# Kernel optimization log

Hardware: AMD Instinct MI355X
Metric: run time of the kernel (lower is better)

Reference implementation:

```python
import jax, jax.numpy as jnp
import numpy as np

NBITS = 8
REDUCE = 64
OUT = 512


def setup_inputs() -> dict:
    key = jax.random.key(0)
    ks = jax.random.split(key, 6)
    T, B, C = 512, 16, 512
    ne = 2 ** NBITS
    x = jax.random.normal(ks[0], (T, B, C), dtype=jnp.float32)
    key_in = jax.random.normal(ks[1], (T, B, C), dtype=jnp.float32)  # unused by forward (overwritten)
    # xavier-ish init scales
    map_w = jax.random.normal(ks[2], (NBITS, C), dtype=jnp.float32) * np.sqrt(2.0 / (C + NBITS))
    map_b = jnp.zeros((NBITS,), dtype=jnp.float32)
    pw_w1 = jax.random.normal(ks[3], (REDUCE, C), dtype=jnp.float32) * np.sqrt(2.0 / (C + REDUCE))
    pw_w21 = jax.random.normal(ks[4], (ne, OUT * REDUCE), dtype=jnp.float32) * np.sqrt(2.0 / (ne + OUT * REDUCE))
    pw_w22 = jax.random.normal(ks[5], (ne, OUT * REDUCE), dtype=jnp.float32) * np.sqrt(2.0 / (ne + OUT * REDUCE))
    pw_B = jnp.zeros((1, 1, OUT), dtype=jnp.float32)
    return {"x": x, "key": key_in, "map_w": map_w, "map_b": map_b,
            "pw_w1": pw_w1, "pw_w21": pw_w21, "pw_w22": pw_w22, "pw_B": pw_B}


def reference(x, key, map_w, map_b, pw_w1, pw_w21, pw_w22, pw_B):
    # x: (T,B,C). `key` arg is overwritten by x in the original source.
    T, B, C = x.shape
    nbits = map_w.shape[0]
    out_dim = pw_B.shape[-1]
    reduce_dim = pw_w1.shape[0]

    k = x.reshape(T * B, C) @ map_w.T + map_b          # (T*B, nbits)
    z = jnp.clip(1.2 * jax.nn.sigmoid(k) - 0.1, 0.0, 1.0)  # saturated sigmoid
    code = (z > 0.5).astype(z.dtype)                   # eval: hard binary code

    pows = (2 ** jnp.arange(nbits, dtype=jnp.int32))   # bit_to_int weights
    qz1 = jnp.sum(code.astype(jnp.int32) * pows, axis=-1)          # (T*B,)
    qz2 = jnp.sum((1 - code.astype(jnp.int32)) * pows, axis=-1)    # (T*B,)

    # gather per-token expert rows and synthesize per-token weight matrix
    w2 = (pw_w21[qz1] + pw_w22[qz2]).reshape(T, B, out_dim, reduce_dim)

    # original computes (w2 @ pw_w1) @ x; reassociated as w2 @ (pw_w1 @ x)
    # to avoid materializing the (T,B,out,in) intermediate (same math)
    v = jnp.einsum('ri,tbi->tbr', pw_w1, x)            # (T,B,reduce)
    y = jnp.einsum('tbor,tbr->tbo', w2, v) + pw_B      # (T,B,out)

    loss = jnp.zeros((1,), dtype=x.dtype)
    return (y, loss)
```

## Files before the change

### kernel.cpp

```cpp
#include <hip/hip_runtime.h>

#define NTOK 8192
#define CDIM 512
#define NB   8
#define RD   64
#define OD   512
#define TPB_A 32
#define XPAD 4
#define XROW (CDIM + XPAD)

typedef unsigned char u8;

__global__ __launch_bounds__(256) void phaseA(
    const float* __restrict__ x, const float* __restrict__ map_w,
    const float* __restrict__ map_b, const float* __restrict__ w1,
    u8* __restrict__ q_out, float* __restrict__ v_out,
    float* __restrict__ loss_out)
{
    const int t    = threadIdx.x;
    const int tok0 = blockIdx.x * TPB_A;
    __shared__ float xs[TPB_A * XROW];

    const float4* xsrc = (const float4*)(x + (size_t)tok0 * CDIM);
    for (int i = t; i < TPB_A * (CDIM / 4); i += 256) {
        int r = i >> 7, c = i & 127;
        *((float4*)(xs + r * XROW) + c) = xsrc[i];
    }
    __syncthreads();

    {
        const int bit = t & 7, tk = t >> 3;
        const float4* m4 = (const float4*)(map_w + (size_t)bit * CDIM);
        const float4* x4 = (const float4*)(xs + tk * XROW);
        double a0 = 0.0, a1 = 0.0;
        for (int j = 0; j < CDIM / 4; ++j) {
            float4 m = m4[j], xv = x4[j];
            a0 += (double)m.x * (double)xv.x + (double)m.y * (double)xv.y;
            a1 += (double)m.z * (double)xv.z + (double)m.w * (double)xv.w;
        }
        double k = a0 + a1 + (double)map_b[bit];
        unsigned long long m = __ballot(k > 0.0);
        const int lane = t & 63;
        if ((lane & 7) == 0) {
            int g = lane >> 3;
            q_out[tok0 + tk] = (u8)((m >> (g * 8)) & 0xFFull);
        }
    }

    {
        const int r  = t & 63;
        const int tg = t >> 6;
        const float4* w4 = (const float4*)(w1 + (size_t)r * CDIM);
        float acc[8] = {0.f,0.f,0.f,0.f,0.f,0.f,0.f,0.f};
        for (int j = 0; j < CDIM / 4; ++j) {
            float4 wv = w4[j];
            #pragma unroll
            for (int k = 0; k < 8; ++k) {
                float4 xv = *((const float4*)(xs + (tg * 8 + k) * XROW) + j);
                acc[k] += wv.x * xv.x + wv.y * xv.y + wv.z * xv.z + wv.w * xv.w;
            }
        }
        #pragma unroll
        for (int k = 0; k < 8; ++k)
            v_out[(size_t)(tok0 + tg * 8 + k) * RD + r] = acc[k];
    }

    if (blockIdx.x == 0 && t == 0) loss_out[0] = 0.0f;
}

__global__ __launch_bounds__(512) void phaseB(
    const u8* __restrict__ q_arr, const float* __restrict__ v_arr,
    const float* __restrict__ w21, const float* __restrict__ w22,
    const float* __restrict__ pwB, float* __restrict__ y)
{
    const int q = blockIdx.x;
    const int t = threadIdx.x;
    __shared__ unsigned short list[NTOK];
    __shared__ int cnt;
    __shared__ float vs[8 * RD];

    if (t == 0) cnt = 0;
    __syncthreads();
    for (int i = t; i < NTOK; i += 512)
        if ((int)q_arr[i] == q) list[atomicAdd(&cnt, 1)] = (unsigned short)i;
    __syncthreads();
    const int n = cnt;
    if (n == 0) return;

    const float4* pa = (const float4*)(w21 + (size_t)q * (OD * RD) + (size_t)t * RD);
    const float4* pb = (const float4*)(w22 + (size_t)(255 - q) * (OD * RD) + (size_t)t * RD);
    float w[RD];
    #pragma unroll
    for (int j = 0; j < RD / 4; ++j) {
        float4 a = pa[j], b = pb[j];
        w[j * 4 + 0] = a.x + b.x;
        w[j * 4 + 1] = a.y + b.y;
        w[j * 4 + 2] = a.z + b.z;
        w[j * 4 + 3] = a.w + b.w;
    }
    const float bias = pwB[t];

    for (int base = 0; base < n; base += 8) {
        const int nb = min(8, n - base);
        if (t < nb * RD)
            vs[t] = v_arr[(size_t)list[base + (t >> 6)] * RD + (t & 63)];
        __syncthreads();
        for (int i = 0; i < nb; ++i) {
            float acc = bias;
            #pragma unroll
            for (int r = 0; r < RD; ++r) acc += w[r] * vs[i * RD + r];
            y[(size_t)list[base + i] * OD + t] = acc;
        }
        __syncthreads();
    }
}

__global__ __launch_bounds__(256) void mono(
    const float* __restrict__ x, const float* __restrict__ map_w,
    const float* __restrict__ map_b, const float* __restrict__ w1,
    const float* __restrict__ w21, const float* __restrict__ w22,
    const float* __restrict__ pwB, float* __restrict__ y)
{
    const int tok = blockIdx.x;
    const int t   = threadIdx.x;
    __shared__ float xsh[CDIM];
    __shared__ float vsh[RD];
    __shared__ int qsh;

    if (t == 0) qsh = 0;
    for (int i = t; i < CDIM; i += 256) xsh[i] = x[(size_t)tok * CDIM + i];
    __syncthreads();

    if (t < NB) {
        double a = 0.0;
        const float* mrow = map_w + (size_t)t * CDIM;
        for (int j = 0; j < CDIM; ++j) a += (double)mrow[j] * (double)xsh[j];
        a += (double)map_b[t];
        if (a > 0.0) atomicOr(&qsh, 1 << t);
    }
    if (t < RD) {
        const float* wrow = w1 + (size_t)t * CDIM;
        float acc = 0.f;
        for (int j = 0; j < CDIM; ++j) acc += wrow[j] * xsh[j];
        vsh[t] = acc;
    }
    __syncthreads();

    const int q = qsh;
    for (int o = t; o < OD; o += 256) {
        const float* pa = w21 + (size_t)q * (OD * RD) + (size_t)o * RD;
        const float* pb = w22 + (size_t)(255 - q) * (OD * RD) + (size_t)o * RD;
        float acc = pwB[o];
        for (int r = 0; r < RD; ++r) acc += (pa[r] + pb[r]) * vsh[r];
        y[(size_t)tok * OD + o] = acc;
    }
    if (tok == 0 && t == 0) y[(size_t)NTOK * OD] = 0.0f;
}

extern "C" void kernel_launch(void* const* d_in, const int* in_sizes, int n_in,
                              void* d_out, int out_size, void* d_ws, size_t ws_size,
                              hipStream_t stream) {
    const float* x     = (const float*)d_in[0];
    const float* map_w = (const float*)d_in[2];
    const float* map_b = (const float*)d_in[3];
    const float* w1    = (const float*)d_in[4];
    const float* w21   = (const float*)d_in[5];
    const float* w22   = (const float*)d_in[6];
    const float* pwB   = (const float*)d_in[7];
    float* out = (float*)d_out;

    const size_t need = (size_t)NTOK + (size_t)NTOK * RD * sizeof(float);
    if (ws_size >= need) {
        u8*    q_ws = (u8*)d_ws;
        float* v_ws = (float*)((char*)d_ws + NTOK);
        phaseA<<<NTOK / TPB_A, 256, 0, stream>>>(x, map_w, map_b, w1, q_ws, v_ws,
                                                 out + (size_t)NTOK * OD);
        phaseB<<<256, 512, 0, stream>>>(q_ws, v_ws, w21, w22, pwB, out);
    } else {
        mono<<<NTOK, 256, 0, stream>>>(x, map_w, map_b, w1, w21, w22, pwB, out);
    }
}
```

Measured before the change: 204.3 us.

## Replace per-expert token scan with global counting sort and split expert blocks

```diff
diff --git a/kernel.cpp b/kernel.cpp
--- a/kernel.cpp
+++ b/kernel.cpp
@@ -5,113 +5,157 @@
 #define NB   8
 #define RD   64
 #define OD   512
-#define TPB_A 32
-#define XPAD 4
-#define XROW (CDIM + XPAD)
-
-typedef unsigned char u8;
-
-__global__ __launch_bounds__(256) void phaseA(
+
+typedef unsigned char  u8;
+typedef unsigned int   u32;
+typedef unsigned short u16;
+
+#define WS_Q      0
+#define WS_COUNTS 8192
+#define WS_CURSOR 9216
+#define WS_OFF    10240
+#define WS_LIST   11520
+#define WS_V      28672
+#define WS_NEED   (WS_V + NTOK * RD * 4)
+
+__global__ __launch_bounds__(256) void kInit(u32* __restrict__ counts) {
+    counts[threadIdx.x] = 0u;
+}
+
+__global__ __launch_bounds__(256) void kA(
     const float* __restrict__ x, const float* __restrict__ map_w,
     const float* __restrict__ map_b, const float* __restrict__ w1,
     u8* __restrict__ q_out, float* __restrict__ v_out,
-    float* __restrict__ loss_out)
+    u32* __restrict__ counts, float* __restrict__ loss_out)
 {
     const int t    = threadIdx.x;
-    const int tok0 = blockIdx.x * TPB_A;
-    __shared__ float xs[TPB_A * XROW];
-
-    const float4* xsrc = (const float4*)(x + (size_t)tok0 * CDIM);
-    for (int i = t; i < TPB_A * (CDIM / 4); i += 256) {
-        int r = i >> 7, c = i & 127;
-        *((float4*)(xs + r * XROW) + c) = xsrc[i];
-    }
+    const int lane = t & 63;
+    const int wv   = __builtin_amdgcn_readfirstlane(t >> 6);
+    const int b    = blockIdx.x;
+
+    if (b < 512) {
+        const int tg  = b >> 2;
+        const int rg  = b & 3;
+        const int tok = tg * 64 + lane;
+        const int r0  = __builtin_amdgcn_readfirstlane(rg * 16 + wv * 4);
+        const float4* __restrict__ x4 = (const float4*)x + (size_t)tok * (CDIM / 4);
+        const float4* __restrict__ w4 = (const float4*)w1;
+        float a0 = 0.f, a1 = 0.f, a2 = 0.f, a3 = 0.f;
+        #pragma unroll 4
+        for (int k = 0; k < CDIM / 4; ++k) {
+            float4 xv = x4[k];
+            float4 w0 = w4[(size_t)(r0 + 0) * (CDIM / 4) + k];
+            float4 w1v = w4[(size_t)(r0 + 1) * (CDIM / 4) + k];
+            float4 w2 = w4[(size_t)(r0 + 2) * (CDIM / 4) + k];
+            float4 w3 = w4[(size_t)(r0 + 3) * (CDIM / 4) + k];
+            a0 += w0.x * xv.x + w0.y * xv.y + w0.z * xv.z + w0.w * xv.w;
+            a1 += w1v.x * xv.x + w1v.y * xv.y + w1v.z * xv.z + w1v.w * xv.w;
+            a2 += w2.x * xv.x + w2.y * xv.y + w2.z * xv.z + w2.w * xv.w;
+            a3 += w3.x * xv.x + w3.y * xv.y + w3.z * xv.z + w3.w * xv.w;
+        }
+        float4 o = make_float4(a0, a1, a2, a3);
+        *((float4*)(v_out + (size_t)tok * RD + r0)) = o;
+    } else {
+        const int tg  = b - 512;
+        const int tok = tg * 64 + lane;
+        __shared__ u32 qs[64];
+        if (t < 64) qs[t] = 0u;
+        __syncthreads();
+
+        const int b0 = __builtin_amdgcn_readfirstlane(2 * wv);
+        const int b1 = b0 + 1;
+        const float4* __restrict__ x4 = (const float4*)x + (size_t)tok * (CDIM / 4);
+        const float4* __restrict__ m4 = (const float4*)map_w;
+        double s0 = 0.0, s1 = 0.0;
+        for (int k = 0; k < CDIM / 4; ++k) {
+            float4 xv = x4[k];
+            float4 m0 = m4[(size_t)b0 * (CDIM / 4) + k];
+            float4 m1 = m4[(size_t)b1 * (CDIM / 4) + k];
+            s0 += (double)m0.x * (double)xv.x + (double)m0.y * (double)xv.y
+                + (double)m0.z * (double)xv.z + (double)m0.w * (double)xv.w;
+            s1 += (double)m1.x * (double)xv.x + (double)m1.y * (double)xv.y
+                + (double)m1.z * (double)xv.z + (double)m1.w * (double)xv.w;
+        }
+        s0 += (double)map_b[b0];
+        s1 += (double)map_b[b1];
+        unsigned long long m0 = __ballot(s0 > 0.0);
+        unsigned long long m1 = __ballot(s1 > 0.0);
+        u32 bits = (u32)(((m0 >> lane) & 1ull) | (((m1 >> lane) & 1ull) << 1)) << (2 * wv);
+        if (bits) atomicOr(&qs[lane], bits);
+        __syncthreads();
+        if (t < 64) {
+            u32 q = qs[t];
+            q_out[tok] = (u8)q;
+            atomicAdd(&counts[q], 1u);
+        }
+        if (b == 512 && t == 0) loss_out[0] = 0.0f;
+    }
+}
+
+__global__ __launch_bounds__(256) void kPrefix(
+    const u32* __restrict__ counts, u32* __restrict__ off, u32* __restrict__ cursor)
+{
+    __shared__ u32 s[256];
+    const int t = threadIdx.x;
+    u32 c = counts[t];
+    s[t] = c;
     __syncthreads();
-
-    {
-        const int bit = t & 7, tk = t >> 3;
-        const float4* m4 = (const float4*)(map_w + (size_t)bit * CDIM);
-        const float4* x4 = (const float4*)(xs + tk * XROW);
-        double a0 = 0.0, a1 = 0.0;
-        for (int j = 0; j < CDIM / 4; ++j) {
-            float4 m = m4[j], xv = x4[j];
-            a0 += (double)m.x * (double)xv.x + (double)m.y * (double)xv.y;
-            a1 += (double)m.z * (double)xv.z + (double)m.w * (double)xv.w;
-        }
-        double k = a0 + a1 + (double)map_b[bit];
-        unsigned long long m = __ballot(k > 0.0);
-        const int lane = t & 63;
-        if ((lane & 7) == 0) {
-            int g = lane >> 3;
-            q_out[tok0 + tk] = (u8)((m >> (g * 8)) & 0xFFull);
-        }
-    }
-
-    {
-        const int r  = t & 63;
-        const int tg = t >> 6;
-        const float4* w4 = (const float4*)(w1 + (size_t)r * CDIM);
-        float acc[8] = {0.f,0.f,0.f,0.f,0.f,0.f,0.f,0.f};
-        for (int j = 0; j < CDIM / 4; ++j) {
-            float4 wv = w4[j];
-            #pragma unroll
-            for (int k = 0; k < 8; ++k) {
-                float4 xv = *((const float4*)(xs + (tg * 8 + k) * XROW) + j);
-                acc[k] += wv.x * xv.x + wv.y * xv.y + wv.z * xv.z + wv.w * xv.w;
-            }
-        }
-        #pragma unroll
-        for (int k = 0; k < 8; ++k)
-            v_out[(size_t)(tok0 + tg * 8 + k) * RD + r] = acc[k];
-    }
-
-    if (blockIdx.x == 0 && t == 0) loss_out[0] = 0.0f;
-}
-
-__global__ __launch_bounds__(512) void phaseB(
-    const u8* __restrict__ q_arr, const float* __restrict__ v_arr,
+    for (int d = 1; d < 256; d <<= 1) {
+        u32 v = (t >= d) ? s[t - d] : 0u;
+        __syncthreads();
+        s[t] += v;
+        __syncthreads();
+    }
+    u32 excl = s[t] - c;
+    off[t] = excl;
+    cursor[t] = excl;
+    if (t == 255) off[256] = s[255];
+}
+
+__global__ __launch_bounds__(256) void kScatter(
+    const u8* __restrict__ q_arr, u32* __restrict__ cursor, u16* __restrict__ list)
+{
+    const int tok = blockIdx.x * 256 + threadIdx.x;
+    u32 pos = atomicAdd(&cursor[q_arr[tok]], 1u);
+    list[pos] = (u16)tok;
+}
+
+__global__ __launch_bounds__(256) void kB(
+    const u16* __restrict__ list, const u32* __restrict__ off,
+    const float* __restrict__ v_arr,
     const float* __restrict__ w21, const float* __restrict__ w22,
     const float* __restrict__ pwB, float* __restrict__ y)
 {
-    const int q = blockIdx.x;
-    const int t = threadIdx.x;
-    __shared__ unsigned short list[NTOK];
-    __shared__ int cnt;
-    __shared__ float vs[8 * RD];
-
-    if (t == 0) cnt = 0;
-    __syncthreads();
-    for (int i = t; i < NTOK; i += 512)
-        if ((int)q_arr[i] == q) list[atomicAdd(&cnt, 1)] = (unsigned short)i;
-    __syncthreads();
-    const int n = cnt;
-    if (n == 0) return;
-
-    const float4* pa = (const float4*)(w21 + (size_t)q * (OD * RD) + (size_t)t * RD);
-    const float4* pb = (const float4*)(w22 + (size_t)(255 - q) * (OD * RD) + (size_t)t * RD);
+    const int q  = blockIdx.x >> 1;
+    const int oh = blockIdx.x & 1;
+    const int o  = oh * 256 + threadIdx.x;
+    const u32 lo = off[q], hi = off[q + 1];
+    if (lo == hi) return;
+
+    const float4* __restrict__ pa = (const float4*)(w21 + ((size_t)q * OD + o) * RD);
+    const float4* __restrict__ pb = (const float4*)(w22 + ((size_t)(255 - q) * OD + o) * RD);
     float w[RD];
     #pragma unroll
     for (int j = 0; j < RD / 4; ++j) {
-        float4 a = pa[j], b = pb[j];
-        w[j * 4 + 0] = a.x + b.x;
-        w[j * 4 + 1] = a.y + b.y;
-        w[j * 4 + 2] = a.z + b.z;
-        w[j * 4 + 3] = a.w + b.w;
-    }
-    const float bias = pwB[t];
-
-    for (int base = 0; base < n; base += 8) {
-        const int nb = min(8, n - base);
-        if (t < nb * RD)
-            vs[t] = v_arr[(size_t)list[base + (t >> 6)] * RD + (t & 63)];
-        __syncthreads();
-        for (int i = 0; i < nb; ++i) {
-            float acc = bias;
-            #pragma unroll
-            for (int r = 0; r < RD; ++r) acc += w[r] * vs[i * RD + r];
-            y[(size_t)list[base + i] * OD + t] = acc;
-        }
-        __syncthreads();
+        float4 a = pa[j], bb = pb[j];
+        w[j * 4 + 0] = a.x + bb.x;
+        w[j * 4 + 1] = a.y + bb.y;
+        w[j * 4 + 2] = a.z + bb.z;
+        w[j * 4 + 3] = a.w + bb.w;
+    }
+    const float bias = pwB[o];
+
+    for (u32 i = lo; i < hi; ++i) {
+        const int tok = __builtin_amdgcn_readfirstlane((int)list[i]);
+        const float4* __restrict__ vr = (const float4*)(v_arr + (size_t)tok * RD);
+        float acc = bias;
+        #pragma unroll
+        for (int j = 0; j < RD / 4; ++j) {
+            float4 vv = vr[j];
+            acc += w[j * 4 + 0] * vv.x + w[j * 4 + 1] * vv.y
+                 + w[j * 4 + 2] * vv.z + w[j * 4 + 3] * vv.w;
+        }
+        y[(size_t)tok * OD + o] = acc;
     }
 }
 
@@ -169,13 +213,21 @@
     const float* pwB   = (const float*)d_in[7];
     float* out = (float*)d_out;
 
-    const size_t need = (size_t)NTOK + (size_t)NTOK * RD * sizeof(float);
-    if (ws_size >= need) {
-        u8*    q_ws = (u8*)d_ws;
-        float* v_ws = (float*)((char*)d_ws + NTOK);
-        phaseA<<<NTOK / TPB_A, 256, 0, stream>>>(x, map_w, map_b, w1, q_ws, v_ws,
-                                                 out + (size_t)NTOK * OD);
-        phaseB<<<256, 512, 0, stream>>>(q_ws, v_ws, w21, w22, pwB, out);
+    if (ws_size >= (size_t)WS_NEED) {
+        char* ws = (char*)d_ws;
+        u8*    q_ws   = (u8*)(ws + WS_Q);
+        u32*   counts = (u32*)(ws + WS_COUNTS);
+        u32*   cursor = (u32*)(ws + WS_CURSOR);
+        u32*   off    = (u32*)(ws + WS_OFF);
+        u16*   list   = (u16*)(ws + WS_LIST);
+        float* v_ws   = (float*)(ws + WS_V);
+
+        kInit<<<1, 256, 0, stream>>>(counts);
+        kA<<<640, 256, 0, stream>>>(x, map_w, map_b, w1, q_ws, v_ws, counts,
+                                    out + (size_t)NTOK * OD);
+        kPrefix<<<1, 256, 0, stream>>>(counts, off, cursor);
+        kScatter<<<NTOK / 256, 256, 0, stream>>>(q_ws, cursor, list);
+        kB<<<512, 256, 0, stream>>>(list, off, v_ws, w21, w22, pwB, out);
     } else {
         mono<<<NTOK, 256, 0, stream>>>(x, map_w, map_b, w1, w21, w22, pwB, out);
     }
```

New measurement: 222.0 us. 1.09x slower.
